# Kernel optimization log

Hardware: AMD Instinct MI355X
Metric: run time of the kernel (lower is better)

Reference implementation:

```python
import jax, jax.numpy as jnp
import numpy as np
from jax import lax

B, N_PROP, N_GT = 8, 8000, 256
NUM_CLASSES = 2
IMG_H = IMG_W = 800.0
FG_T = BG_T = 0.5            # Matcher thresholds
WX, WY, WW, WH = 10.0, 10.0, 5.0, 5.0  # BoxCoder weights
SCORE_T, NMS_T = 0.05, 0.5
PRE_NMS, DETS = 1000, 300     # boxes entering NMS, detections_per_img
DW_CLIP = float(np.log(1000.0 / 16.0))


def _rand_boxes(key, shape):
    k1, k2, k3, k4 = jax.random.split(key, 4)
    x1 = jax.random.uniform(k1, shape) * (IMG_W - 60.0)
    y1 = jax.random.uniform(k2, shape) * (IMG_H - 60.0)
    w = 10.0 + jax.random.uniform(k3, shape) * 250.0
    h = 10.0 + jax.random.uniform(k4, shape) * 250.0
    return jnp.stack([x1, y1, jnp.minimum(x1 + w, IMG_W), jnp.minimum(y1 + h, IMG_H)], -1)


def setup_inputs() -> dict:
    key = jax.random.key(0)
    kp, kg, kl, kb = jax.random.split(key, 4)
    n_all = N_PROP + N_GT
    return {
        "proposals": _rand_boxes(kp, (B, N_PROP)),
        "gt_boxes": _rand_boxes(kg, (B, N_GT)),
        "logits": jax.random.normal(kl, (B, n_all, NUM_CLASSES), jnp.float32),
        "box_regression": jax.random.normal(kb, (B, n_all, NUM_CLASSES * 4), jnp.float32) * 0.1,
    }


def box_iou(a, b):
    # a: [Na,4], b: [Nb,4] in xyxy -> [Na,Nb]
    area_a = (a[:, 2] - a[:, 0]) * (a[:, 3] - a[:, 1])
    area_b = (b[:, 2] - b[:, 0]) * (b[:, 3] - b[:, 1])
    lt = jnp.maximum(a[:, None, :2], b[None, :, :2])
    rb = jnp.minimum(a[:, None, 2:], b[None, :, 2:])
    wh = jnp.clip(rb - lt, 0.0)
    inter = wh[..., 0] * wh[..., 1]
    return inter / (area_a[:, None] + area_b[None, :] - inter)


def encode(ref_boxes, gt):
    # BoxCoder.encode, weights (10,10,5,5)
    pw = ref_boxes[:, 2] - ref_boxes[:, 0]
    ph = ref_boxes[:, 3] - ref_boxes[:, 1]
    pcx = ref_boxes[:, 0] + 0.5 * pw
    pcy = ref_boxes[:, 1] + 0.5 * ph
    gw = gt[:, 2] - gt[:, 0]
    gh = gt[:, 3] - gt[:, 1]
    gcx = gt[:, 0] + 0.5 * gw
    gcy = gt[:, 1] + 0.5 * gh
    return jnp.stack([
        WX * (gcx - pcx) / pw,
        WY * (gcy - pcy) / ph,
        WW * jnp.log(gw / pw),
        WH * jnp.log(gh / ph),
    ], -1)


def decode(rel, boxes):
    # rel: [N, C*4], boxes: [N,4] -> [N, C, 4]
    rel = rel.reshape(rel.shape[0], -1, 4)
    pw = boxes[:, 2] - boxes[:, 0]
    ph = boxes[:, 3] - boxes[:, 1]
    pcx = boxes[:, 0] + 0.5 * pw
    pcy = boxes[:, 1] + 0.5 * ph
    dx = rel[..., 0] / WX
    dy = rel[..., 1] / WY
    dw = jnp.minimum(rel[..., 2] / WW, DW_CLIP)
    dh = jnp.minimum(rel[..., 3] / WH, DW_CLIP)
    cx = dx * pw[:, None] + pcx[:, None]
    cy = dy * ph[:, None] + pcy[:, None]
    w = jnp.exp(dw) * pw[:, None]
    h = jnp.exp(dh) * ph[:, None]
    return jnp.stack([cx - 0.5 * w, cy - 0.5 * h, cx + 0.5 * w, cy + 0.5 * h], -1)


def _per_image(prop, gt, logit, breg):
    n_all = prop.shape[0] + gt.shape[0]
    prop_all = jnp.concatenate([prop, gt], 0)  # select_training_samples concat

    # --- assign_targets_to_proposals (Matcher) ---
    iou = box_iou(gt, prop_all)                 # [G, N_all]
    vals = iou.max(0)
    matches = iou.argmax(0)
    # gt_labels are all 1; bg -> 0, between thresholds -> -1 (empty when fg==bg)
    labels = jnp.where(vals < BG_T, 0, jnp.where(vals < FG_T, -1, 1))
    matched_gt = gt[matches]                    # [N_all, 4]
    reg_targets = encode(prop_all, matched_gt)  # [N_all, 4]

    # --- postprocess_detections ---
    pred = decode(breg, prop_all)               # [N_all, C, 4]
    boxes1 = pred[:, 1, :]                      # drop background class
    boxes1 = jnp.stack([
        jnp.clip(boxes1[:, 0], 0.0, IMG_W),
        jnp.clip(boxes1[:, 1], 0.0, IMG_H),
        jnp.clip(boxes1[:, 2], 0.0, IMG_W),
        jnp.clip(boxes1[:, 3], 0.0, IMG_H),
    ], -1)
    scores = jax.nn.softmax(logit, -1)[:, 1]
    sc = jnp.where(scores > SCORE_T, scores, -1.0)  # score_thresh filter

    top_s, top_i = lax.top_k(sc, PRE_NMS)
    top_b = boxes1[top_i]                       # [M, 4]
    ious = box_iou(top_b, top_b)                # [M, M]
    idx = jnp.arange(PRE_NMS)

    def body(keep, i):
        sup = (ious[i] > NMS_T) & keep[i] & (idx > i)
        return keep & ~sup, None

    keep, _ = lax.scan(body, jnp.ones(PRE_NMS, bool), idx)
    final = jnp.where(keep & (top_s > 0.0), top_s, -1.0)
    det_s, sel = lax.top_k(final, DETS)
    det_b = top_b[sel]
    return labels.astype(jnp.float32), reg_targets, det_b, det_s


def reference(proposals, gt_boxes, logits, box_regression):
    return jax.vmap(_per_image)(proposals, gt_boxes, logits, box_regression)
```

## Files before the change

### kernel.cpp

```cpp
#include <hip/hip_runtime.h>
#include <math.h>

#pragma clang fp contract(off)

#define BATCH 8
#define N_PROP 8000
#define N_GT 256
#define N_ALL 8256
#define PRE_NMS 1000
#define DETS 300
#define IMG 800.0f
#define DW_CLIP 4.135166556742356f
#define NWORDS 32
#define NBINS 8192
#define BIN_SCALE 8192.0f
#define MASK_BLOCKS 125
#define PREP_BLOCKS 258

__device__ __forceinline__ float exf(float x) { return (float)exp((double)x); }
__device__ __forceinline__ float lgf(float x) { return (float)log((double)x); }

__device__ __forceinline__ int score_bin(float s) {
  int b = (int)(s * BIN_SCALE);
  return (b < 0) ? 0 : (b > NBINS - 1 ? NBINS - 1 : b);
}

__device__ __forceinline__ int bxp(int j) { return j ^ ((j >> 5) & 7); }

#define REP32(F) F(0) F(1) F(2) F(3) F(4) F(5) F(6) F(7) F(8) F(9) F(10) \
  F(11) F(12) F(13) F(14) F(15) F(16) F(17) F(18) F(19) F(20) F(21) F(22) \
  F(23) F(24) F(25) F(26) F(27) F(28) F(29) F(30) F(31)


__global__ void __launch_bounds__(1024)
select_rank_kernel(const float* __restrict__ prop,
                   const float* __restrict__ gt,
                   const float* __restrict__ logits,
                   const float* __restrict__ breg,
                   float* __restrict__ top_s,
                   float* __restrict__ top_b) {
  const int b = blockIdx.x;
  const int tid = threadIdx.x;
  const int lane = tid & 63, wid = tid >> 6;
  __shared__ __align__(16) float ssc[N_ALL];
  __shared__ unsigned hist[NBINS];
  __shared__ __align__(16) float sc2[N_ALL];
  __shared__ unsigned short idx2[N_ALL];
  __shared__ __align__(16) float4 gsh[N_GT];
  __shared__ int s_wt[16], s_wx[16];
  __shared__ int s_T, s_Nc;

  if (tid < N_GT) gsh[tid] = ((const float4*)(gt + (size_t)b * N_GT * 4))[tid];

  for (int k = tid; k < N_ALL; k += 1024) {
    const float2 lg = *(const float2*)(logits + ((size_t)b * N_ALL + k) * 2);
    const float m = fmaxf(lg.x, lg.y);
    const float e0 = exf(lg.x - m), e1 = exf(lg.y - m);
    const float s = e1 / (e0 + e1);
    ssc[k] = (s > 0.05f) ? s : -1.0f;
  }
  #pragma unroll
  for (int i = 0; i < NBINS / 1024; ++i) hist[tid + i * 1024] = 0u;
  __syncthreads();
  for (int k = tid; k < N_ALL; k += 1024)
    atomicAdd(&hist[score_bin(ssc[k])], 1u);
  __syncthreads();

  int local = 0;
  #pragma unroll
  for (int i = 0; i < NBINS / 1024; ++i) local += (int)hist[tid * (NBINS / 1024) + i];

  int incl = local;
  #pragma unroll
  for (int off = 1; off < 64; off <<= 1) {
    const int u = __shfl_down(incl, off);
    incl += (lane + off < 64) ? u : 0;
  }
  if (lane == 0) s_wt[wid] = incl;
  __syncthreads();
  if (tid < 16) {
    const int v = s_wt[tid];
    int inc2 = v;
    #pragma unroll
    for (int off = 1; off < 16; off <<= 1) {
      const int u = __shfl_down(inc2, off);
      inc2 += (tid + off < 16) ? u : 0;
    }
    s_wx[tid] = inc2 - v;
  }
  __syncthreads();
  const int sa = (incl - local) + s_wx[wid];

  {
    int above = sa;
    const int hi = tid * (NBINS / 1024) + (NBINS / 1024) - 1;
    #pragma unroll
    for (int i = 0; i < NBINS / 1024; ++i) {
      const int bin = hi - i;
      const int c = (int)hist[bin];
      if (above < PRE_NMS && above + c >= PRE_NMS) { s_T = bin; s_Nc = above + c; }
      hist[bin] = (unsigned)above;
      above += c;
    }
  }
  __syncthreads();
  const int T = s_T;
  const int Nc = s_Nc;

  for (int k = tid; k < N_ALL; k += 1024) {
    const float v = ssc[k];
    const int bb = score_bin(v);
    if (bb >= T) {
      const int slot = (int)atomicAdd(&hist[bb], 1u);
      sc2[slot] = v;
      idx2[slot] = (unsigned short)k;
    }
  }
  __syncthreads();

  float* tsb = top_s + (size_t)b * PRE_NMS;
  float4* tbb = (float4*)top_b + (size_t)b * PRE_NMS;
  for (int s = tid; s < Nc; s += 1024) {
    const float my = sc2[s];
    const int myb = score_bin(my);
    const int myi = (int)idx2[s];
    int gl = s;
    while (gl > 0 && score_bin(sc2[gl - 1]) == myb) --gl;
    int rank = gl;
    for (int k2 = gl; k2 < Nc; ++k2) {
      const float v = sc2[k2];
      if (score_bin(v) != myb) break;
      if (k2 == s) continue;
      rank += (int)((v > my) | ((v == my) & ((int)idx2[k2] < myi)));
    }
    if (rank < PRE_NMS) {
      tsb[rank] = my;
      float4 pb;
      if (myi < N_PROP) pb = ((const float4*)(prop + (size_t)b * N_PROP * 4))[myi];
      else              pb = gsh[myi - N_PROP];
      const float pw = pb.z - pb.x, ph = pb.w - pb.y;
      const float pcx = pb.x + 0.5f * pw, pcy = pb.y + 0.5f * ph;
      const float4 r = *(const float4*)(breg + (((size_t)b * N_ALL + myi) * 8 + 4));
      const float dx = r.x / 10.0f, dy = r.y / 10.0f;
      const float dw = fminf(r.z / 5.0f, DW_CLIP);
      const float dh = fminf(r.w / 5.0f, DW_CLIP);
      const float cx = dx * pw + pcx, cy = dy * ph + pcy;
      const float w2 = exf(dw) * pw, h2 = exf(dh) * ph;
      float4 bb;
      bb.x = fminf(fmaxf(cx - 0.5f * w2, 0.0f), IMG);
      bb.y = fminf(fmaxf(cy - 0.5f * h2, 0.0f), IMG);
      bb.z = fminf(fmaxf(cx + 0.5f * w2, 0.0f), IMG);
      bb.w = fminf(fmaxf(cy + 0.5f * h2, 0.0f), IMG);
      tbb[rank] = bb;
    }
  }
}

__global__ void __launch_bounds__(256)
mask_prep_kernel(const float* __restrict__ prop,
                 const float* __restrict__ gt,
                 const float* __restrict__ top_b,
                 unsigned* __restrict__ ws_mask,
                 float* __restrict__ out_labels,
                 float* __restrict__ out_regt) {
  const int b = blockIdx.y;
  const int tid = threadIdx.x;
  __shared__ __align__(16) float4 bx[PRE_NMS];
  __shared__ __align__(16) float4 gsh4[N_GT];
  __shared__ float s_best[32];
  __shared__ int s_bi[32];

  if (blockIdx.x < MASK_BLOCKS) {
    {
      const float4* gb = (const float4*)top_b + (size_t)b * PRE_NMS;
      float4 v0 = gb[tid], v1 = gb[tid + 256], v2 = gb[tid + 512];
      float4 v3 = make_float4(0.f, 0.f, 0.f, 0.f);
      const bool g3 = (tid + 768) < PRE_NMS;
      if (g3) v3 = gb[tid + 768];
      bx[bxp(tid)] = v0; bx[bxp(tid + 256)] = v1; bx[bxp(tid + 512)] = v2;
      if (g3) bx[bxp(tid + 768)] = v3;
    }
    __syncthreads();
    const int idx = blockIdx.x * 256 + tid;
    const int i = idx >> 5;
    const int w = idx & 31;
    const float4 bi = bx[bxp(i)];
    const float ai = (bi.z - bi.x) * (bi.w - bi.y);
    unsigned bits = 0u;
    const int j0 = w * 32;
    #pragma unroll 8
    for (int jj = 0; jj < 32; ++jj) {
      const int j = j0 + jj;
      if (j > i && j < PRE_NMS) {
        const float4 bj = bx[bxp(j)];
        const float aj = (bj.z - bj.x) * (bj.w - bj.y);
        const float ww = fmaxf(fminf(bi.z, bj.z) - fmaxf(bi.x, bj.x), 0.0f);
        const float hh = fmaxf(fminf(bi.w, bj.w) - fmaxf(bi.y, bj.y), 0.0f);
        const float inter = ww * hh;
        const float iou = inter / (ai + aj - inter);
        if (iou > 0.5f) bits |= (1u << jj);
      }
    }
    ws_mask[((size_t)b * PRE_NMS + i) * NWORDS + w] = bits;
  } else {
    {
      const float4* g4 = (const float4*)(gt + (size_t)b * N_GT * 4);
      gsh4[tid] = g4[tid];
    }
    __syncthreads();

    const int grp = tid >> 3;
    const int gl  = tid & 7;
    const int j = (blockIdx.x - MASK_BLOCKS) * 32 + grp;

    float x1, y1, x2, y2;
    if (j < N_PROP) {
      const float4 p = ((const float4*)(prop + (size_t)b * N_PROP * 4))[j];
      x1 = p.x; y1 = p.y; x2 = p.z; y2 = p.w;
    } else {
      const float4 g = gsh4[j - N_PROP];
      x1 = g.x; y1 = g.y; x2 = g.z; y2 = g.w;
    }
    const float areaP = (x2 - x1) * (y2 - y1);

    float best = -1.0f; int bi = gl;
    #pragma unroll 4
    for (int t = 0; t < 32; ++t) {
      const int i = gl + (t << 3);
      const float4 g = gsh4[i];
      const float ga = (g.z - g.x) * (g.w - g.y);
      const float w = fmaxf(fminf(g.z, x2) - fmaxf(g.x, x1), 0.0f);
      const float h = fmaxf(fminf(g.w, y2) - fmaxf(g.y, y1), 0.0f);
      const float inter = w * h;
      const float iou = inter / (ga + areaP - inter);
      if (iou > best) { best = iou; bi = i; }
    }
    #pragma unroll
    for (int m = 1; m < 8; m <<= 1) {
      const float ov = __shfl_xor(best, m, 64);
      const int   oi = __shfl_xor(bi,  m, 64);
      if (ov > best || (ov == best && oi < bi)) { best = ov; bi = oi; }
    }
    if (gl == 0) { s_best[grp] = best; s_bi[grp] = bi; }
    __syncthreads();

    if (tid < 32) {
      const int j2 = (blockIdx.x - MASK_BLOCKS) * 32 + tid;
      const float bst = s_best[tid];
      const int   gi  = s_bi[tid];

      float px1, py1, px2, py2;
      if (j2 < N_PROP) {
        const float4 p = ((const float4*)(prop + (size_t)b * N_PROP * 4))[j2];
        px1 = p.x; py1 = p.y; px2 = p.z; py2 = p.w;
      } else {
        const float4 g = gsh4[j2 - N_PROP];
        px1 = g.x; py1 = g.y; px2 = g.z; py2 = g.w;
      }

      out_labels[(size_t)b * N_ALL + j2] = (bst < 0.5f) ? 0.0f : 1.0f;

      const float pw = px2 - px1, ph = py2 - py1;
      const float pcx = px1 + 0.5f * pw, pcy = py1 + 0.5f * ph;
      const float4 gb = gsh4[gi];
      const float gw = gb.z - gb.x, gh = gb.w - gb.y;
      const float gcx = gb.x + 0.5f * gw, gcy = gb.y + 0.5f * gh;
      float4 rt;
      rt.x = 10.0f * (gcx - pcx) / pw;
      rt.y = 10.0f * (gcy - pcy) / ph;
      rt.z = 5.0f * lgf(gw / pw);
      rt.w = 5.0f * lgf(gh / ph);
      ((float4*)out_regt)[(size_t)b * N_ALL + j2] = rt;
    }
  }
}

__global__ void __launch_bounds__(256)
scan_kernel(const unsigned* __restrict__ ws_mask,
            const float* __restrict__ top_s,
            const float* __restrict__ top_b,
            float* __restrict__ out_detb,
            float* __restrict__ out_dets) {
  const int b = blockIdx.x;
  const int tid = threadIdx.x;
  __shared__ __align__(16) unsigned smask[PRE_NMS * NWORDS];
  __shared__ int s_npos;
  __shared__ unsigned s_flw[NWORDS];
  __shared__ int s_pref[NWORDS + 1];
  const float* ts = top_s + (size_t)b * PRE_NMS;

  if (tid == 0) s_npos = 0;
  {
    const uint4* gm = (const uint4*)(ws_mask + (size_t)b * PRE_NMS * NWORDS);
    uint4* sm4 = (uint4*)smask;
    #pragma unroll
    for (int gs = 0; gs < 4; ++gs) {
      const int k0 = gs * 2048 + tid;
      uint4 t0 = gm[k0],        t1 = gm[k0 + 256],  t2 = gm[k0 + 512];
      uint4 t3 = gm[k0 + 768],  t4 = gm[k0 + 1024], t5 = gm[k0 + 1280];
      uint4 t6 = gm[k0 + 1536];
      uint4 t7 = make_uint4(0u, 0u, 0u, 0u);
      const bool g7 = (k0 + 1792) < (PRE_NMS * NWORDS / 4);
      if (g7) t7 = gm[k0 + 1792];
      sm4[k0] = t0;        sm4[k0 + 256] = t1;  sm4[k0 + 512] = t2;
      sm4[k0 + 768] = t3;  sm4[k0 + 1024] = t4; sm4[k0 + 1280] = t5;
      sm4[k0 + 1536] = t6;
      if (g7) sm4[k0 + 1792] = t7;
    }
  }
  int cnt = 0;
  for (int k = tid; k < PRE_NMS; k += 256) cnt += (ts[k] > 0.0f) ? 1 : 0;
  __syncthreads();
  if (cnt) atomicAdd(&s_npos, cnt);

  unsigned keep = 0u;
  if (tid < 64) {
    const int lane = tid;
    const int lw = lane & 31;
    keep = (lane < NWORDS) ? ((lane == 31) ? 0xFFu : 0xFFFFFFFFu) : 0u;
#define DECLA(J) unsigned rA##J;
    REP32(DECLA)
#undef DECLA
    for (int win = 0; win < 32; ++win) {
      unsigned sw = (unsigned)__builtin_amdgcn_readlane((int)keep, win);
      if (sw) {
        const int base = win * 32;
#define LOADA(J) rA##J = smask[(base + J) * NWORDS + lw];
        REP32(LOADA)
#undef LOADA
        unsigned sup = 0u;
#define STEPJ(J) { \
        const unsigned mJ = 0u - ((sw >> J) & 1u); \
        const unsigned rwJ = (unsigned)__builtin_amdgcn_readlane((int)rA##J, win); \
        sw &= ~(rwJ & mJ); \
        sup |= (rA##J & mJ); }
        REP32(STEPJ)
#undef STEPJ
        keep &= ~sup;
      }
    }
  }
  __syncthreads();
  const int n_pos = s_npos;
  if (tid < NWORDS) {
    const int lo = tid * 32;
    int np = n_pos - lo;
    np = (np < 0) ? 0 : (np > 32 ? 32 : np);
    const unsigned npm = (np >= 32) ? 0xFFFFFFFFu : ((1u << np) - 1u);
    s_flw[tid] = keep & npm;
  }
  __syncthreads();
  if (tid == 0) {
    int s = 0;
    #pragma unroll
    for (int w = 0; w < NWORDS; ++w) { s_pref[w] = s; s += __popc(s_flw[w]); }
    s_pref[NWORDS] = s;
  }
  __syncthreads();
  const int tot = s_pref[NWORDS];

  for (int k = tid; k < PRE_NMS; k += 256) {
    const unsigned fw = s_flw[k >> 5];
    const int fbit = (int)((fw >> (k & 31)) & 1u);
    const int pos = s_pref[k >> 5] + __popc(fw & ((1u << (k & 31)) - 1u));
    int slot = -1; float sval = 0.0f;
    if (fbit) {
      if (pos < DETS) { slot = pos; sval = ts[k]; }
    } else {
      const int s2 = tot + (k - pos);
      if (s2 < DETS) { slot = s2; sval = -1.0f; }
    }
    if (slot >= 0) {
      out_dets[(size_t)b * DETS + slot] = sval;
      ((float4*)out_detb)[(size_t)b * DETS + slot] =
          ((const float4*)top_b)[(size_t)b * PRE_NMS + k];
    }
  }
}

extern "C" void kernel_launch(void* const* d_in, const int* in_sizes, int n_in,
                              void* d_out, int out_size, void* d_ws, size_t ws_size,
                              hipStream_t stream) {
  const float* prop   = (const float*)d_in[0];
  const float* gt     = (const float*)d_in[1];
  const float* logits = (const float*)d_in[2];
  const float* breg   = (const float*)d_in[3];

  float* out        = (float*)d_out;
  float* out_labels = out;
  float* out_regt   = out + (size_t)BATCH * N_ALL;
  float* out_detb   = out_regt + (size_t)BATCH * N_ALL * 4;
  float* out_dets   = out_detb + (size_t)BATCH * DETS * 4;

  float* ws_tops   = (float*)d_ws;
  float* ws_topb   = ws_tops + (size_t)BATCH * PRE_NMS;
  unsigned* ws_mask = (unsigned*)(ws_topb + (size_t)BATCH * PRE_NMS * 4);

  hipLaunchKernelGGL(select_rank_kernel, dim3(BATCH), dim3(1024), 0, stream,
                     prop, gt, logits, breg, ws_tops, ws_topb);
  hipLaunchKernelGGL(mask_prep_kernel,
                     dim3(MASK_BLOCKS + PREP_BLOCKS, BATCH), dim3(256), 0, stream,
                     prop, gt, ws_topb, ws_mask, out_labels, out_regt);
  hipLaunchKernelGGL(scan_kernel, dim3(BATCH), dim3(256), 0, stream,
                     ws_mask, ws_tops, ws_topb, out_detb, out_dets);
}
```

Before: 66.63 us.

## Overlap matcher prep with top-k selection and early-exit NMS scan at DETS kept

```diff
diff --git a/kernel.cpp b/kernel.cpp
--- a/kernel.cpp
+++ b/kernel.cpp
@@ -14,8 +14,8 @@
 #define NWORDS 32
 #define NBINS 8192
 #define BIN_SCALE 8192.0f
-#define MASK_BLOCKS 125
-#define PREP_BLOCKS 258
+#define PREP_PER_BATCH 65
+#define SEL_BLOCKS 8
 
 __device__ __forceinline__ float exf(float x) { return (float)exp((double)x); }
 __device__ __forceinline__ float lgf(float x) { return (float)log((double)x); }
@@ -33,15 +33,16 @@
 
 
 __global__ void __launch_bounds__(1024)
-select_rank_kernel(const float* __restrict__ prop,
-                   const float* __restrict__ gt,
-                   const float* __restrict__ logits,
-                   const float* __restrict__ breg,
-                   float* __restrict__ top_s,
-                   float* __restrict__ top_b) {
-  const int b = blockIdx.x;
+fused_select_prep_kernel(const float* __restrict__ prop,
+                         const float* __restrict__ gt,
+                         const float* __restrict__ logits,
+                         const float* __restrict__ breg,
+                         float* __restrict__ out_labels,
+                         float* __restrict__ out_regt,
+                         float* __restrict__ top_s,
+                         float* __restrict__ top_b) {
+  const int idx = blockIdx.x;
   const int tid = threadIdx.x;
-  const int lane = tid & 63, wid = tid >> 6;
   __shared__ __align__(16) float ssc[N_ALL];
   __shared__ unsigned hist[NBINS];
   __shared__ __align__(16) float sc2[N_ALL];
@@ -49,176 +50,143 @@
   __shared__ __align__(16) float4 gsh[N_GT];
   __shared__ int s_wt[16], s_wx[16];
   __shared__ int s_T, s_Nc;
-
-  if (tid < N_GT) gsh[tid] = ((const float4*)(gt + (size_t)b * N_GT * 4))[tid];
-
-  for (int k = tid; k < N_ALL; k += 1024) {
-    const float2 lg = *(const float2*)(logits + ((size_t)b * N_ALL + k) * 2);
-    const float m = fmaxf(lg.x, lg.y);
-    const float e0 = exf(lg.x - m), e1 = exf(lg.y - m);
-    const float s = e1 / (e0 + e1);
-    ssc[k] = (s > 0.05f) ? s : -1.0f;
-  }
-  #pragma unroll
-  for (int i = 0; i < NBINS / 1024; ++i) hist[tid + i * 1024] = 0u;
-  __syncthreads();
-  for (int k = tid; k < N_ALL; k += 1024)
-    atomicAdd(&hist[score_bin(ssc[k])], 1u);
-  __syncthreads();
-
-  int local = 0;
-  #pragma unroll
-  for (int i = 0; i < NBINS / 1024; ++i) local += (int)hist[tid * (NBINS / 1024) + i];
-
-  int incl = local;
-  #pragma unroll
-  for (int off = 1; off < 64; off <<= 1) {
-    const int u = __shfl_down(incl, off);
-    incl += (lane + off < 64) ? u : 0;
-  }
-  if (lane == 0) s_wt[wid] = incl;
-  __syncthreads();
-  if (tid < 16) {
-    const int v = s_wt[tid];
-    int inc2 = v;
-    #pragma unroll
-    for (int off = 1; off < 16; off <<= 1) {
-      const int u = __shfl_down(inc2, off);
-      inc2 += (tid + off < 16) ? u : 0;
-    }
-    s_wx[tid] = inc2 - v;
-  }
-  __syncthreads();
-  const int sa = (incl - local) + s_wx[wid];
-
-  {
-    int above = sa;
-    const int hi = tid * (NBINS / 1024) + (NBINS / 1024) - 1;
-    #pragma unroll
-    for (int i = 0; i < NBINS / 1024; ++i) {
-      const int bin = hi - i;
-      const int c = (int)hist[bin];
-      if (above < PRE_NMS && above + c >= PRE_NMS) { s_T = bin; s_Nc = above + c; }
-      hist[bin] = (unsigned)above;
-      above += c;
-    }
-  }
-  __syncthreads();
-  const int T = s_T;
-  const int Nc = s_Nc;
-
-  for (int k = tid; k < N_ALL; k += 1024) {
-    const float v = ssc[k];
-    const int bb = score_bin(v);
-    if (bb >= T) {
-      const int slot = (int)atomicAdd(&hist[bb], 1u);
-      sc2[slot] = v;
-      idx2[slot] = (unsigned short)k;
-    }
-  }
-  __syncthreads();
-
-  float* tsb = top_s + (size_t)b * PRE_NMS;
-  float4* tbb = (float4*)top_b + (size_t)b * PRE_NMS;
-  for (int s = tid; s < Nc; s += 1024) {
-    const float my = sc2[s];
-    const int myb = score_bin(my);
-    const int myi = (int)idx2[s];
-    int gl = s;
-    while (gl > 0 && score_bin(sc2[gl - 1]) == myb) --gl;
-    int rank = gl;
-    for (int k2 = gl; k2 < Nc; ++k2) {
-      const float v = sc2[k2];
-      if (score_bin(v) != myb) break;
-      if (k2 == s) continue;
-      rank += (int)((v > my) | ((v == my) & ((int)idx2[k2] < myi)));
-    }
-    if (rank < PRE_NMS) {
-      tsb[rank] = my;
-      float4 pb;
-      if (myi < N_PROP) pb = ((const float4*)(prop + (size_t)b * N_PROP * 4))[myi];
-      else              pb = gsh[myi - N_PROP];
-      const float pw = pb.z - pb.x, ph = pb.w - pb.y;
-      const float pcx = pb.x + 0.5f * pw, pcy = pb.y + 0.5f * ph;
-      const float4 r = *(const float4*)(breg + (((size_t)b * N_ALL + myi) * 8 + 4));
-      const float dx = r.x / 10.0f, dy = r.y / 10.0f;
-      const float dw = fminf(r.z / 5.0f, DW_CLIP);
-      const float dh = fminf(r.w / 5.0f, DW_CLIP);
-      const float cx = dx * pw + pcx, cy = dy * ph + pcy;
-      const float w2 = exf(dw) * pw, h2 = exf(dh) * ph;
-      float4 bb;
-      bb.x = fminf(fmaxf(cx - 0.5f * w2, 0.0f), IMG);
-      bb.y = fminf(fmaxf(cy - 0.5f * h2, 0.0f), IMG);
-      bb.z = fminf(fmaxf(cx + 0.5f * w2, 0.0f), IMG);
-      bb.w = fminf(fmaxf(cy + 0.5f * h2, 0.0f), IMG);
-      tbb[rank] = bb;
-    }
-  }
-}
-
-__global__ void __launch_bounds__(256)
-mask_prep_kernel(const float* __restrict__ prop,
-                 const float* __restrict__ gt,
-                 const float* __restrict__ top_b,
-                 unsigned* __restrict__ ws_mask,
-                 float* __restrict__ out_labels,
-                 float* __restrict__ out_regt) {
-  const int b = blockIdx.y;
-  const int tid = threadIdx.x;
-  __shared__ __align__(16) float4 bx[PRE_NMS];
   __shared__ __align__(16) float4 gsh4[N_GT];
-  __shared__ float s_best[32];
-  __shared__ int s_bi[32];
-
-  if (blockIdx.x < MASK_BLOCKS) {
+  __shared__ float s_best[128];
+  __shared__ int s_bi[128];
+
+  if (idx < SEL_BLOCKS) {
+    const int b = idx;
+    const int lane = tid & 63, wid = tid >> 6;
+
+    if (tid < N_GT) gsh[tid] = ((const float4*)(gt + (size_t)b * N_GT * 4))[tid];
+
+    for (int k = tid; k < N_ALL; k += 1024) {
+      const float2 lg = *(const float2*)(logits + ((size_t)b * N_ALL + k) * 2);
+      const float m = fmaxf(lg.x, lg.y);
+      const float e0 = exf(lg.x - m), e1 = exf(lg.y - m);
+      const float s = e1 / (e0 + e1);
+      ssc[k] = (s > 0.05f) ? s : -1.0f;
+    }
+    #pragma unroll
+    for (int i = 0; i < NBINS / 1024; ++i) hist[tid + i * 1024] = 0u;
+    __syncthreads();
+    for (int k = tid; k < N_ALL; k += 1024)
+      atomicAdd(&hist[score_bin(ssc[k])], 1u);
+    __syncthreads();
+
+    int local = 0;
+    #pragma unroll
+    for (int i = 0; i < NBINS / 1024; ++i) local += (int)hist[tid * (NBINS / 1024) + i];
+
+    int incl = local;
+    #pragma unroll
+    for (int off = 1; off < 64; off <<= 1) {
+      const int u = __shfl_down(incl, off);
+      incl += (lane + off < 64) ? u : 0;
+    }
+    if (lane == 0) s_wt[wid] = incl;
+    __syncthreads();
+    if (tid < 16) {
+      const int v = s_wt[tid];
+      int inc2 = v;
+      #pragma unroll
+      for (int off = 1; off < 16; off <<= 1) {
+        const int u = __shfl_down(inc2, off);
+        inc2 += (tid + off < 16) ? u : 0;
+      }
+      s_wx[tid] = inc2 - v;
+    }
+    __syncthreads();
+    const int sa = (incl - local) + s_wx[wid];
+
     {
-      const float4* gb = (const float4*)top_b + (size_t)b * PRE_NMS;
-      float4 v0 = gb[tid], v1 = gb[tid + 256], v2 = gb[tid + 512];
-      float4 v3 = make_float4(0.f, 0.f, 0.f, 0.f);
-      const bool g3 = (tid + 768) < PRE_NMS;
-      if (g3) v3 = gb[tid + 768];
-      bx[bxp(tid)] = v0; bx[bxp(tid + 256)] = v1; bx[bxp(tid + 512)] = v2;
-      if (g3) bx[bxp(tid + 768)] = v3;
-    }
-    __syncthreads();
-    const int idx = blockIdx.x * 256 + tid;
-    const int i = idx >> 5;
-    const int w = idx & 31;
-    const float4 bi = bx[bxp(i)];
-    const float ai = (bi.z - bi.x) * (bi.w - bi.y);
-    unsigned bits = 0u;
-    const int j0 = w * 32;
-    #pragma unroll 8
-    for (int jj = 0; jj < 32; ++jj) {
-      const int j = j0 + jj;
-      if (j > i && j < PRE_NMS) {
-        const float4 bj = bx[bxp(j)];
-        const float aj = (bj.z - bj.x) * (bj.w - bj.y);
-        const float ww = fmaxf(fminf(bi.z, bj.z) - fmaxf(bi.x, bj.x), 0.0f);
-        const float hh = fmaxf(fminf(bi.w, bj.w) - fmaxf(bi.y, bj.y), 0.0f);
-        const float inter = ww * hh;
-        const float iou = inter / (ai + aj - inter);
-        if (iou > 0.5f) bits |= (1u << jj);
-      }
-    }
-    ws_mask[((size_t)b * PRE_NMS + i) * NWORDS + w] = bits;
+      int above = sa;
+      const int hi = tid * (NBINS / 1024) + (NBINS / 1024) - 1;
+      #pragma unroll
+      for (int i = 0; i < NBINS / 1024; ++i) {
+        const int bin = hi - i;
+        const int c = (int)hist[bin];
+        if (above < PRE_NMS && above + c >= PRE_NMS) { s_T = bin; s_Nc = above + c; }
+        hist[bin] = (unsigned)above;
+        above += c;
+      }
+    }
+    __syncthreads();
+    const int T = s_T;
+    const int Nc = s_Nc;
+
+    for (int k = tid; k < N_ALL; k += 1024) {
+      const float v = ssc[k];
+      const int bb = score_bin(v);
+      if (bb >= T) {
+        const int slot = (int)atomicAdd(&hist[bb], 1u);
+        sc2[slot] = v;
+        idx2[slot] = (unsigned short)k;
+      }
+    }
+    __syncthreads();
+
+    float* tsb = top_s + (size_t)b * PRE_NMS;
+    float4* tbb = (float4*)top_b + (size_t)b * PRE_NMS;
+    for (int s = tid; s < Nc; s += 1024) {
+      const float my = sc2[s];
+      const int myb = score_bin(my);
+      const int myi = (int)idx2[s];
+      int gl = s;
+      while (gl > 0 && score_bin(sc2[gl - 1]) == myb) --gl;
+      int rank = gl;
+      for (int k2 = gl; k2 < Nc; ++k2) {
+        const float v = sc2[k2];
+        if (score_bin(v) != myb) break;
+        if (k2 == s) continue;
+        rank += (int)((v > my) | ((v == my) & ((int)idx2[k2] < myi)));
+      }
+      if (rank < PRE_NMS) {
+        tsb[rank] = my;
+        float4 pb;
+        if (myi < N_PROP) pb = ((const float4*)(prop + (size_t)b * N_PROP * 4))[myi];
+        else              pb = gsh[myi - N_PROP];
+        const float pw = pb.z - pb.x, ph = pb.w - pb.y;
+        const float pcx = pb.x + 0.5f * pw, pcy = pb.y + 0.5f * ph;
+        const float4 r = *(const float4*)(breg + (((size_t)b * N_ALL + myi) * 8 + 4));
+        const float dx = r.x / 10.0f, dy = r.y / 10.0f;
+        const float dw = fminf(r.z / 5.0f, DW_CLIP);
+        const float dh = fminf(r.w / 5.0f, DW_CLIP);
+        const float cx = dx * pw + pcx, cy = dy * ph + pcy;
+        const float w2 = exf(dw) * pw, h2 = exf(dh) * ph;
+        float4 bb;
+        bb.x = fminf(fmaxf(cx - 0.5f * w2, 0.0f), IMG);
+        bb.y = fminf(fmaxf(cy - 0.5f * h2, 0.0f), IMG);
+        bb.z = fminf(fmaxf(cx + 0.5f * w2, 0.0f), IMG);
+        bb.w = fminf(fmaxf(cy + 0.5f * h2, 0.0f), IMG);
+        tbb[rank] = bb;
+      }
+    }
   } else {
+    const int pbx = idx - SEL_BLOCKS;
+    const int b = pbx / PREP_PER_BATCH;
+    const int blk = pbx - b * PREP_PER_BATCH;
     {
-      const float4* g4 = (const float4*)(gt + (size_t)b * N_GT * 4);
-      gsh4[tid] = g4[tid];
+      if (tid < N_GT)
+        gsh4[tid] = ((const float4*)(gt + (size_t)b * N_GT * 4))[tid];
     }
     __syncthreads();
 
     const int grp = tid >> 3;
     const int gl  = tid & 7;
-    const int j = (blockIdx.x - MASK_BLOCKS) * 32 + grp;
+    const int j0b = blk * 128;
+    const int j = j0b + grp;
+    const bool jv = (j < N_ALL);
 
     float x1, y1, x2, y2;
-    if (j < N_PROP) {
+    if (jv && j < N_PROP) {
       const float4 p = ((const float4*)(prop + (size_t)b * N_PROP * 4))[j];
       x1 = p.x; y1 = p.y; x2 = p.z; y2 = p.w;
+    } else if (jv) {
+      const float4 g = gsh4[j - N_PROP];
+      x1 = g.x; y1 = g.y; x2 = g.z; y2 = g.w;
     } else {
-      const float4 g = gsh4[j - N_PROP];
+      const float4 g = gsh4[0];
       x1 = g.x; y1 = g.y; x2 = g.z; y2 = g.w;
     }
     const float areaP = (x2 - x1) * (y2 - y1);
@@ -244,35 +212,76 @@
     if (gl == 0) { s_best[grp] = best; s_bi[grp] = bi; }
     __syncthreads();
 
-    if (tid < 32) {
-      const int j2 = (blockIdx.x - MASK_BLOCKS) * 32 + tid;
-      const float bst = s_best[tid];
-      const int   gi  = s_bi[tid];
-
-      float px1, py1, px2, py2;
-      if (j2 < N_PROP) {
-        const float4 p = ((const float4*)(prop + (size_t)b * N_PROP * 4))[j2];
-        px1 = p.x; py1 = p.y; px2 = p.z; py2 = p.w;
-      } else {
-        const float4 g = gsh4[j2 - N_PROP];
-        px1 = g.x; py1 = g.y; px2 = g.z; py2 = g.w;
-      }
-
-      out_labels[(size_t)b * N_ALL + j2] = (bst < 0.5f) ? 0.0f : 1.0f;
-
-      const float pw = px2 - px1, ph = py2 - py1;
-      const float pcx = px1 + 0.5f * pw, pcy = py1 + 0.5f * ph;
-      const float4 gb = gsh4[gi];
-      const float gw = gb.z - gb.x, gh = gb.w - gb.y;
-      const float gcx = gb.x + 0.5f * gw, gcy = gb.y + 0.5f * gh;
-      float4 rt;
-      rt.x = 10.0f * (gcx - pcx) / pw;
-      rt.y = 10.0f * (gcy - pcy) / ph;
-      rt.z = 5.0f * lgf(gw / pw);
-      rt.w = 5.0f * lgf(gh / ph);
-      ((float4*)out_regt)[(size_t)b * N_ALL + j2] = rt;
-    }
-  }
+    if (tid < 128) {
+      const int j2 = j0b + tid;
+      if (j2 < N_ALL) {
+        const float bst = s_best[tid];
+        const int   gi  = s_bi[tid];
+
+        float px1, py1, px2, py2;
+        if (j2 < N_PROP) {
+          const float4 p = ((const float4*)(prop + (size_t)b * N_PROP * 4))[j2];
+          px1 = p.x; py1 = p.y; px2 = p.z; py2 = p.w;
+        } else {
+          const float4 g = gsh4[j2 - N_PROP];
+          px1 = g.x; py1 = g.y; px2 = g.z; py2 = g.w;
+        }
+
+        out_labels[(size_t)b * N_ALL + j2] = (bst < 0.5f) ? 0.0f : 1.0f;
+
+        const float pw = px2 - px1, ph = py2 - py1;
+        const float pcx = px1 + 0.5f * pw, pcy = py1 + 0.5f * ph;
+        const float4 gb = gsh4[gi];
+        const float gw = gb.z - gb.x, gh = gb.w - gb.y;
+        const float gcx = gb.x + 0.5f * gw, gcy = gb.y + 0.5f * gh;
+        float4 rt;
+        rt.x = 10.0f * (gcx - pcx) / pw;
+        rt.y = 10.0f * (gcy - pcy) / ph;
+        rt.z = 5.0f * lgf(gw / pw);
+        rt.w = 5.0f * lgf(gh / ph);
+        ((float4*)out_regt)[(size_t)b * N_ALL + j2] = rt;
+      }
+    }
+  }
+}
+
+__global__ void mask_kernel(const float* __restrict__ top_b,
+                            unsigned* __restrict__ ws_mask) {
+  const int b = blockIdx.y;
+  __shared__ __align__(16) float4 bx[PRE_NMS];
+  const int tid = threadIdx.x;
+  {
+    const float4* gb = (const float4*)top_b + (size_t)b * PRE_NMS;
+    float4 v0 = gb[tid], v1 = gb[tid + 256], v2 = gb[tid + 512];
+    float4 v3 = make_float4(0.f, 0.f, 0.f, 0.f);
+    const bool g3 = (tid + 768) < PRE_NMS;
+    if (g3) v3 = gb[tid + 768];
+    bx[bxp(tid)] = v0; bx[bxp(tid + 256)] = v1; bx[bxp(tid + 512)] = v2;
+    if (g3) bx[bxp(tid + 768)] = v3;
+  }
+  __syncthreads();
+  const int idx = blockIdx.x * blockDim.x + tid;
+  if (idx >= PRE_NMS * NWORDS) return;
+  const int i = idx >> 5;
+  const int w = idx & 31;
+  const float4 bi = bx[bxp(i)];
+  const float ai = (bi.z - bi.x) * (bi.w - bi.y);
+  unsigned bits = 0u;
+  const int j0 = w * 32;
+  #pragma unroll 8
+  for (int jj = 0; jj < 32; ++jj) {
+    const int j = j0 + jj;
+    if (j > i && j < PRE_NMS) {
+      const float4 bj = bx[bxp(j)];
+      const float aj = (bj.z - bj.x) * (bj.w - bj.y);
+      const float ww = fmaxf(fminf(bi.z, bj.z) - fmaxf(bi.x, bj.x), 0.0f);
+      const float hh = fmaxf(fminf(bi.w, bj.w) - fmaxf(bi.y, bj.y), 0.0f);
+      const float inter = ww * hh;
+      const float iou = inter / (ai + aj - inter);
+      if (iou > 0.5f) bits |= (1u << jj);
+    }
+  }
+  ws_mask[((size_t)b * PRE_NMS + i) * NWORDS + w] = bits;
 }
 
 __global__ void __launch_bounds__(256)
@@ -312,6 +321,8 @@
   for (int k = tid; k < PRE_NMS; k += 256) cnt += (ts[k] > 0.0f) ? 1 : 0;
   __syncthreads();
   if (cnt) atomicAdd(&s_npos, cnt);
+  __syncthreads();
+  const int n_pos = s_npos;
 
   unsigned keep = 0u;
   if (tid < 64) {
@@ -321,6 +332,7 @@
 #define DECLA(J) unsigned rA##J;
     REP32(DECLA)
 #undef DECLA
+    int c300 = 0;
     for (int win = 0; win < 32; ++win) {
       unsigned sw = (unsigned)__builtin_amdgcn_readlane((int)keep, win);
       if (sw) {
@@ -338,10 +350,14 @@
 #undef STEPJ
         keep &= ~sup;
       }
-    }
-  }
-  __syncthreads();
-  const int n_pos = s_npos;
+      int npw = n_pos - win * 32;
+      npw = (npw < 0) ? 0 : (npw > 32 ? 32 : npw);
+      const unsigned npmw = (npw >= 32) ? 0xFFFFFFFFu : ((1u << npw) - 1u);
+      c300 += __popc(sw & npmw);
+      if (c300 >= DETS) break;
+    }
+  }
+  __syncthreads();
   if (tid < NWORDS) {
     const int lo = tid * 32;
     int np = n_pos - lo;
@@ -396,11 +412,13 @@
   float* ws_topb   = ws_tops + (size_t)BATCH * PRE_NMS;
   unsigned* ws_mask = (unsigned*)(ws_topb + (size_t)BATCH * PRE_NMS * 4);
 
-  hipLaunchKernelGGL(select_rank_kernel, dim3(BATCH), dim3(1024), 0, stream,
-                     prop, gt, logits, breg, ws_tops, ws_topb);
-  hipLaunchKernelGGL(mask_prep_kernel,
-                     dim3(MASK_BLOCKS + PREP_BLOCKS, BATCH), dim3(256), 0, stream,
-                     prop, gt, ws_topb, ws_mask, out_labels, out_regt);
+  hipLaunchKernelGGL(fused_select_prep_kernel,
+                     dim3(SEL_BLOCKS + PREP_PER_BATCH * BATCH), dim3(1024), 0, stream,
+                     prop, gt, logits, breg, out_labels, out_regt,
+                     ws_tops, ws_topb);
+  dim3 gridm((PRE_NMS * NWORDS + 255) / 256, BATCH);
+  hipLaunchKernelGGL(mask_kernel, gridm, dim3(256), 0, stream,
+                     ws_topb, ws_mask);
   hipLaunchKernelGGL(scan_kernel, dim3(BATCH), dim3(256), 0, stream,
                      ws_mask, ws_tops, ws_topb, out_detb, out_dets);
 }
```

New measurement: 56.22 us. -15.6%, faster.
